# Kernel tuning notes

Measured on AMD Instinct MI355X. Metric: run time of the kernel, lower is better.

The kernel has to match this reference:

```python
import jax, jax.numpy as jnp
import numpy as np

NU, NI, D, E = 100000, 50000, 128, 500000


def setup_inputs() -> dict:
    key = jax.random.key(0)
    ks = jax.random.split(key, 10)
    s = 1.0 / np.sqrt(D)
    return {
        "feat_user": jax.random.normal(ks[0], (NU, D), jnp.float32),
        "feat_item": jax.random.normal(ks[1], (NI, D), jnp.float32),
        "W1": jax.random.normal(ks[2], (D, D), jnp.float32) * s,
        "b1": jnp.zeros((D,), jnp.float32),
        "W2": jax.random.normal(ks[3], (D, D), jnp.float32) * s,
        "b2": jnp.zeros((D,), jnp.float32),
        "norm_u2i": jax.random.uniform(ks[4], (E, 1), jnp.float32),
        "norm_i2u": jax.random.uniform(ks[5], (E, 1), jnp.float32),
        "edge_u2i_src": jax.random.randint(ks[6], (E,), 0, NU, jnp.int32),
        "edge_u2i_dst": jax.random.randint(ks[7], (E,), 0, NI, jnp.int32),
        "edge_i2u_src": jax.random.randint(ks[8], (E,), 0, NI, jnp.int32),
        "edge_i2u_dst": jax.random.randint(ks[9], (E,), 0, NU, jnp.int32),
    }


def reference(feat_user, feat_item, W1, b1, W2, b2, norm_u2i, norm_i2u,
              edge_u2i_src, edge_u2i_dst, edge_i2u_src, edge_i2u_dst):
    lin1 = lambda x: x @ W1 + b1
    lin2 = lambda x: x @ W2 + b2

    # self-loop etypes: copy_u(W1(feat)) summed over one self-edge per node
    h_user = lin1(feat_user)
    h_item = lin1(feat_item)

    # user -> item edges: norm * (W1(e_u) + W2(e_u * e_i)), scatter-sum to items
    su = feat_user[edge_u2i_src]            # [E, D]
    di = feat_item[edge_u2i_dst]            # [E, D]
    m_ui = norm_u2i * (lin1(su) + lin2(su * di))
    h_item = h_item + jax.ops.segment_sum(m_ui, edge_u2i_dst, num_segments=feat_item.shape[0])

    # item -> user edges
    si = feat_item[edge_i2u_src]
    du = feat_user[edge_i2u_dst]
    m_iu = norm_i2u * (lin1(si) + lin2(si * du))
    h_user = h_user + jax.ops.segment_sum(m_iu, edge_i2u_dst, num_segments=feat_user.shape[0])

    def finish(h):
        h = jax.nn.leaky_relu(h, 0.2)       # LeakyReLU(0.2); dropout p=0 is identity
        n = jnp.linalg.norm(h, axis=1, keepdims=True)
        return h / jnp.maximum(n, 1e-12)    # F.normalize(dim=1, p=2), eps=1e-12

    return finish(h_user), finish(h_item)
```

## Files before the change

### kernel.cpp

```cpp
#include <hip/hip_runtime.h>

#define DD 128
#define SCAN_TILE 1024
#define HS 132

typedef __attribute__((ext_vector_type(8))) short short8;
typedef __attribute__((ext_vector_type(4))) float f32x4;

__device__ inline unsigned short f2bf_rne(float f) {
    unsigned int u = __float_as_uint(f);
    unsigned int r = u + 0x7FFFu + ((u >> 16) & 1u);
    return (unsigned short)(r >> 16);
}
__device__ inline float bf2f(unsigned short h) {
    return __uint_as_float(((unsigned int)h) << 16);
}
__device__ inline void split2(float a, float b, unsigned int& hi, unsigned int& lo) {
    unsigned short ha = f2bf_rne(a), hb = f2bf_rne(b);
    float la = a - bf2f(ha), lb = b - bf2f(hb);
    hi = (unsigned int)ha | ((unsigned int)hb << 16);
    lo = (unsigned int)f2bf_rne(la) | ((unsigned int)f2bf_rne(lb) << 16);
}


__global__ __launch_bounds__(256) void count_kernel(
    const int* __restrict__ dst1, int E1, int* deg1,
    const int* __restrict__ dst2, int E2, int* deg2)
{
    int t = blockIdx.x * 256 + threadIdx.x;
    if (t < E1) {
        atomicAdd(deg1 + dst1[t], 1);
    } else if (t - E1 < E2) {
        atomicAdd(deg2 + dst2[t - E1], 1);
    }
}

__global__ __launch_bounds__(256) void scanA_kernel(
    const int* __restrict__ cur_i, int NI,
    const int* __restrict__ cur_u, int NU,
    int* bsum, int nb0)
{
    int b = blockIdx.x;
    const int* cur;
    int N, base;
    if (b < nb0) { cur = cur_i; N = NI; base = b * SCAN_TILE; }
    else         { cur = cur_u; N = NU; base = (b - nb0) * SCAN_TILE; }
    int t = threadIdx.x;
    int idx0 = base + t * 4;
    int s = 0;
    #pragma unroll
    for (int k = 0; k < 4; ++k) {
        int idx = idx0 + k;
        if (idx < N) s += cur[idx];
    }
    __shared__ int red[256];
    red[t] = s;
    __syncthreads();
    for (int o = 128; o >= 1; o >>= 1) {
        if (t < o) red[t] += red[t + o];
        __syncthreads();
    }
    if (t == 0) bsum[b] = red[0];
}

__device__ int block_exscan_inplace(int* a, int n)
{
    __shared__ int sh[256];
    int t = threadIdx.x;
    int carry = 0;
    for (int base = 0; base < n; base += 256) {
        int v = (base + t < n) ? a[base + t] : 0;
        sh[t] = v;
        __syncthreads();
        for (int off = 1; off < 256; off <<= 1) {
            int u = (t >= off) ? sh[t - off] : 0;
            __syncthreads();
            sh[t] += u;
            __syncthreads();
        }
        if (base + t < n) a[base + t] = carry + sh[t] - v;
        int csum = sh[255];
        __syncthreads();
        carry += csum;
    }
    return carry;
}

__global__ __launch_bounds__(256) void scanB_kernel(
    int* bsum, int nb0, int nb1,
    int* row_i, int NI, int* row_u, int NU)
{
    int tot0 = block_exscan_inplace(bsum, nb0);
    __syncthreads();
    int tot1 = block_exscan_inplace(bsum + nb0, nb1);
    if (threadIdx.x == 0) {
        row_i[NI] = tot0;
        row_u[NU] = tot1;
    }
}

__global__ __launch_bounds__(256) void scanC_kernel(
    int* cur_i, int* row_i, int NI,
    int* cur_u, int* row_u, int NU,
    const int* __restrict__ bsum, int nb0)
{
    int b = blockIdx.x;
    int off = bsum[b];
    int* cur; int* row;
    int N, base;
    if (b < nb0) { cur = cur_i; row = row_i; N = NI; base = b * SCAN_TILE; }
    else         { cur = cur_u; row = row_u; N = NU; base = (b - nb0) * SCAN_TILE; }
    int t = threadIdx.x;
    int idx0 = base + t * 4;
    int v[4];
    int s = 0;
    #pragma unroll
    for (int k = 0; k < 4; ++k) {
        int idx = idx0 + k;
        v[k] = (idx < N) ? cur[idx] : 0;
        s += v[k];
    }
    __shared__ int sh[256];
    sh[t] = s;
    __syncthreads();
    for (int o = 1; o < 256; o <<= 1) {
        int u = (t >= o) ? sh[t - o] : 0;
        __syncthreads();
        sh[t] += u;
        __syncthreads();
    }
    int run = off + sh[t] - s;
    #pragma unroll
    for (int k = 0; k < 4; ++k) {
        int idx = idx0 + k;
        if (idx < N) {
            row[idx] = run;
            cur[idx] = run;
            run += v[k];
        }
    }
}

__global__ __launch_bounds__(256) void fill_pg_kernel(
    const int* __restrict__ dst1, const int* __restrict__ src1,
    const float* __restrict__ norm1, int E1, int* cur1, int* ss1, float* ns1,
    const int* __restrict__ dst2, const int* __restrict__ src2,
    const float* __restrict__ norm2, int E2, int* cur2, int* ss2, float* ns2)
{
    int t = blockIdx.x * 256 + threadIdx.x;
    if (t < E1) {
        int pos = atomicAdd(cur1 + dst1[t], 1);
        ss1[pos] = src1[t];
        ns1[pos] = norm1[t];
    } else if (t - E1 < E2) {
        int e = t - E1;
        int pos = atomicAdd(cur2 + dst2[e], 1);
        ss2[pos] = src2[e];
        ns2[pos] = norm2[e];
    }
}


__global__ __launch_bounds__(256) void scatter_kernel(
    const float* __restrict__ feat_src,
    const int* __restrict__ src,
    const int* __restrict__ dst,
    const float* __restrict__ norm,
    float* agg,
    float* ssum,
    int E)
{
    int gw = (int)((blockIdx.x * 256u + threadIdx.x) >> 6);
    int lane = threadIdx.x & 63;
    if (gw >= E) return;
    int si = src[gw];
    int di = dst[gw];
    float nv = norm[gw];
    float2 v = *(const float2*)(feat_src + (size_t)si * DD + lane * 2);
    float* ap = agg + (size_t)di * DD + lane * 2;
    unsafeAtomicAdd(ap,     v.x * nv);
    unsafeAtomicAdd(ap + 1, v.y * nv);
    if (lane == 0) unsafeAtomicAdd(ssum + di, nv);
}

__global__ __launch_bounds__(256) void wprep_kernel(
    const float* __restrict__ W1, const float* __restrict__ W2,
    unsigned short* wfrag)
{
    int t = blockIdx.x * 256 + threadIdx.x;
    if (t >= 4096) return;
    int lane = t & 63;
    int cf   = (t >> 6) & 7;
    int ksm  = (t >> 9) & 3;
    int mat  = t >> 11;
    const float* W = mat ? W2 : W1;
    int g = lane >> 4, c = lane & 15;
    int n = cf * 16 + c;
    unsigned int hi[4], lo[4];
    #pragma unroll
    for (int p = 0; p < 4; ++p) {
        int k0 = ksm * 32 + g * 8 + p * 2;
        float v0 = W[(size_t)k0 * DD + n];
        float v1 = W[(size_t)(k0 + 1) * DD + n];
        split2(v0, v1, hi[p], lo[p]);
    }
    unsigned short* dh = wfrag + (size_t)mat * 32768
                       + ((size_t)(ksm * 8 + cf) * 64 + lane) * 8;
    unsigned short* dl = dh + 16384;
    *(uint4*)dh = make_uint4(hi[0], hi[1], hi[2], hi[3]);
    *(uint4*)dl = make_uint4(lo[0], lo[1], lo[2], lo[3]);
}

__global__ __launch_bounds__(256) void fused_kernel(
    const float* __restrict__ feat_user, const float* __restrict__ feat_item,
    const int* __restrict__ row_u, const int* __restrict__ ss2,
    const float* __restrict__ ns2, int NU, int nbU,
    const int* __restrict__ row_i, const int* __restrict__ ss1,
    const float* __restrict__ ns1, int NI,
    const unsigned short* __restrict__ wfrag,
    const float* __restrict__ b1, const float* __restrict__ b2,
    float* out_base)
{
    __shared__ __align__(16) unsigned short Ah[32 * 256];
    __shared__ __align__(16) unsigned short Al[32 * 256];
    __shared__ float sst[32];

    const float *featO, *featS, *ns;
    const int *row, *ss;
    float* out;
    int row0, nrows;
    if ((int)blockIdx.x < nbU) {
        featO = feat_user; featS = feat_item; row = row_u; ss = ss2; ns = ns2;
        out = out_base; row0 = blockIdx.x * 32; nrows = NU;
    } else {
        featO = feat_item; featS = feat_user; row = row_i; ss = ss1; ns = ns1;
        out = out_base + (size_t)NU * DD;
        row0 = (blockIdx.x - nbU) * 32; nrows = NI;
    }

    int t = threadIdx.x;
    int w = t >> 6;
    int lane = t & 63;
    char* pAh = (char*)Ah;
    char* pAl = (char*)Al;

    for (int rr = 0; rr < 8; ++rr) {
        int r = w * 8 + rr;
        int grow = row0 + r;
        float2 acc = {0.f, 0.f};
        float sn = 0.f;
        float2 f2 = {0.f, 0.f};
        if (grow < nrows) {
            f2 = *(const float2*)(featO + (size_t)grow * DD + lane * 2);
            int beg = row[grow], end = row[grow + 1];
            int j = beg;
            for (; j + 4 <= end; j += 4) {
                int s0 = ss[j], s1 = ss[j + 1], s2 = ss[j + 2], s3 = ss[j + 3];
                float n0 = ns[j],     n1 = ns[j + 1];
                float n2 = ns[j + 2], n3 = ns[j + 3];
                float2 v0 = *(const float2*)(featS + (size_t)s0 * DD + lane * 2);
                float2 v1 = *(const float2*)(featS + (size_t)s1 * DD + lane * 2);
                float2 v2 = *(const float2*)(featS + (size_t)s2 * DD + lane * 2);
                float2 v3 = *(const float2*)(featS + (size_t)s3 * DD + lane * 2);
                acc.x += n0 * v0.x + n1 * v1.x + n2 * v2.x + n3 * v3.x;
                acc.y += n0 * v0.y + n1 * v1.y + n2 * v2.y + n3 * v3.y;
                sn += n0 + n1 + n2 + n3;
            }
            for (; j < end; ++j) {
                int s0 = ss[j];
                float n0 = ns[j];
                float2 v0 = *(const float2*)(featS + (size_t)s0 * DD + lane * 2);
                acc.x += n0 * v0.x;
                acc.y += n0 * v0.y;
                sn += n0;
            }
        }
        float x0 = f2.x + acc.x, x1 = f2.y + acc.y;
        float y0 = f2.x * acc.x, y1 = f2.y * acc.y;
        unsigned int xh, xl, yh, yl;
        split2(x0, x1, xh, xl);
        split2(y0, y1, yh, yl);
        int swz = (r & 7) << 4;
        int rb = r * 512;
        int xo = rb + ((4 * lane) ^ swz);
        int yo = rb + ((256 + 4 * lane) ^ swz);
        *(unsigned int*)(pAh + xo) = xh;
        *(unsigned int*)(pAl + xo) = xl;
        *(unsigned int*)(pAh + yo) = yh;
        *(unsigned int*)(pAl + yo) = yl;
        if (lane == 0) sst[r] = sn;
    }
    __syncthreads();

    int r16 = lane & 15, g = lane >> 4;
    f32x4 acc00 = {0.f,0.f,0.f,0.f}, acc01 = {0.f,0.f,0.f,0.f};
    f32x4 acc10 = {0.f,0.f,0.f,0.f}, acc11 = {0.f,0.f,0.f,0.f};
    const char* cAh = (const char*)Ah;
    const char* cAl = (const char*)Al;
    int swzA = (r16 & 7) << 4;
    int ob0 = r16 * 512;
    int ob1 = (r16 + 16) * 512;

    #pragma unroll 2
    for (int ks = 0; ks < 8; ++ks) {
        int kb = ks * 64 + g * 16;
        int offx = kb ^ swzA;
        short8 a0h = *(const short8*)(cAh + ob0 + offx);
        short8 a0l = *(const short8*)(cAl + ob0 + offx);
        short8 a1h = *(const short8*)(cAh + ob1 + offx);
        short8 a1l = *(const short8*)(cAl + ob1 + offx);
        int mat = ks >> 2, ksm = ks & 3;
        const unsigned short* ph = wfrag + (size_t)mat * 32768;
        const unsigned short* pl = ph + 16384;
        int bo0 = ((ksm * 8 + w * 2) * 64 + lane) * 8;
        int bo1 = bo0 + 512;
        short8 b0h = *(const short8*)(ph + bo0);
        short8 b0l = *(const short8*)(pl + bo0);
        short8 b1h = *(const short8*)(ph + bo1);
        short8 b1l = *(const short8*)(pl + bo1);
        acc00 = __builtin_amdgcn_mfma_f32_16x16x32_bf16(a0h, b0h, acc00, 0, 0, 0);
        acc00 = __builtin_amdgcn_mfma_f32_16x16x32_bf16(a0h, b0l, acc00, 0, 0, 0);
        acc00 = __builtin_amdgcn_mfma_f32_16x16x32_bf16(a0l, b0h, acc00, 0, 0, 0);
        acc01 = __builtin_amdgcn_mfma_f32_16x16x32_bf16(a0h, b1h, acc01, 0, 0, 0);
        acc01 = __builtin_amdgcn_mfma_f32_16x16x32_bf16(a0h, b1l, acc01, 0, 0, 0);
        acc01 = __builtin_amdgcn_mfma_f32_16x16x32_bf16(a0l, b1h, acc01, 0, 0, 0);
        acc10 = __builtin_amdgcn_mfma_f32_16x16x32_bf16(a1h, b0h, acc10, 0, 0, 0);
        acc10 = __builtin_amdgcn_mfma_f32_16x16x32_bf16(a1h, b0l, acc10, 0, 0, 0);
        acc10 = __builtin_amdgcn_mfma_f32_16x16x32_bf16(a1l, b0h, acc10, 0, 0, 0);
        acc11 = __builtin_amdgcn_mfma_f32_16x16x32_bf16(a1h, b1h, acc11, 0, 0, 0);
        acc11 = __builtin_amdgcn_mfma_f32_16x16x32_bf16(a1h, b1l, acc11, 0, 0, 0);
        acc11 = __builtin_amdgcn_mfma_f32_16x16x32_bf16(a1l, b1h, acc11, 0, 0, 0);
    }
    __syncthreads();

    float* hbuf = (float*)Ah;
    #pragma unroll
    for (int j = 0; j < 4; ++j) {
        int rA = g * 4 + j;
        hbuf[rA * HS        + (w * 32 + r16)]      = acc00[j];
        hbuf[rA * HS        + (w * 32 + 16 + r16)] = acc01[j];
        hbuf[(16 + rA) * HS + (w * 32 + r16)]      = acc10[j];
        hbuf[(16 + rA) * HS + (w * 32 + 16 + r16)] = acc11[j];
    }
    __syncthreads();

    int c0 = t & 63, c1 = c0 + 64, rg = t >> 6;
    float b1c0 = b1[c0], b1c1 = b1[c1];
    float b2c0 = b2[c0], b2c1 = b2[c1];
    #pragma unroll
    for (int rr = 0; rr < 8; ++rr) {
        int lr = rg * 8 + rr;
        int row_ = row0 + lr;
        if (row_ < nrows) {
            float s = sst[lr];
            float h0 = hbuf[lr * HS + c0] + (1.0f + s) * b1c0 + s * b2c0;
            float h1 = hbuf[lr * HS + c1] + (1.0f + s) * b1c1 + s * b2c1;
            h0 = h0 >= 0.f ? h0 : 0.2f * h0;
            h1 = h1 >= 0.f ? h1 : 0.2f * h1;
            float loc = h0 * h0 + h1 * h1;
            #pragma unroll
            for (int m = 32; m >= 1; m >>= 1) loc += __shfl_xor(loc, m, 64);
            float inv = 1.0f / fmaxf(sqrtf(loc), 1e-12f);
            __builtin_nontemporal_store(h0 * inv, out + (size_t)row_ * DD + c0);
            __builtin_nontemporal_store(h1 * inv, out + (size_t)row_ * DD + c1);
        }
    }
}


__global__ __launch_bounds__(256) void finish_kernel(
    const float* __restrict__ feat,
    const float* agg,
    const float* __restrict__ ssum,
    const float* __restrict__ W1,
    const float* __restrict__ b1,
    const float* __restrict__ W2,
    const float* __restrict__ b2,
    float* out,
    int nrows)
{
    __shared__ float xs[32][DD];
    __shared__ float ys[32][DD];
    int row0 = blockIdx.x * 32;
    int tid = threadIdx.x;

    for (int i = tid; i < 32 * (DD / 4); i += 256) {
        int r = i >> 5;
        int c4 = (i & 31) * 4;
        int row = row0 + r;
        if (row < nrows) {
            float4 f = *(const float4*)(feat + (size_t)row * DD + c4);
            float4 a = *(const float4*)(agg  + (size_t)row * DD + c4);
            float4 x, y;
            x.x = f.x + a.x; x.y = f.y + a.y; x.z = f.z + a.z; x.w = f.w + a.w;
            y.x = f.x * a.x; y.y = f.y * a.y; y.z = f.z * a.z; y.w = f.w * a.w;
            *(float4*)&xs[r][c4] = x;
            *(float4*)&ys[r][c4] = y;
        }
    }
    __syncthreads();

    int c0 = tid & 63;
    int rg = tid >> 6;
    int c1 = c0 + 64;

    float acc[8][2] = {{0.f,0.f},{0.f,0.f},{0.f,0.f},{0.f,0.f},
                       {0.f,0.f},{0.f,0.f},{0.f,0.f},{0.f,0.f}};
    for (int k = 0; k < DD; k += 4) {
        float w1a[4], w1b[4], w2a[4], w2b[4];
        #pragma unroll
        for (int kk = 0; kk < 4; ++kk) {
            const float* wr1 = W1 + (size_t)(k + kk) * DD;
            const float* wr2 = W2 + (size_t)(k + kk) * DD;
            w1a[kk] = wr1[c0]; w1b[kk] = wr1[c1];
            w2a[kk] = wr2[c0]; w2b[kk] = wr2[c1];
        }
        #pragma unroll
        for (int r = 0; r < 8; ++r) {
            float4 xv = *(const float4*)&xs[rg * 8 + r][k];
            float4 yv = *(const float4*)&ys[rg * 8 + r][k];
            acc[r][0] += xv.x*w1a[0] + xv.y*w1a[1] + xv.z*w1a[2] + xv.w*w1a[3]
                       + yv.x*w2a[0] + yv.y*w2a[1] + yv.z*w2a[2] + yv.w*w2a[3];
            acc[r][1] += xv.x*w1b[0] + xv.y*w1b[1] + xv.z*w1b[2] + xv.w*w1b[3]
                       + yv.x*w2b[0] + yv.y*w2b[1] + yv.z*w2b[2] + yv.w*w2b[3];
        }
    }

    float b1c0 = b1[c0], b1c1 = b1[c1];
    float b2c0 = b2[c0], b2c1 = b2[c1];

    #pragma unroll
    for (int r = 0; r < 8; ++r) {
        int row = row0 + rg * 8 + r;
        if (row < nrows) {
            float s = ssum[row];
            float h0 = acc[r][0] + (1.0f + s) * b1c0 + s * b2c0;
            float h1 = acc[r][1] + (1.0f + s) * b1c1 + s * b2c1;
            h0 = h0 >= 0.f ? h0 : 0.2f * h0;
            h1 = h1 >= 0.f ? h1 : 0.2f * h1;
            float loc = h0 * h0 + h1 * h1;
            #pragma unroll
            for (int m = 32; m >= 1; m >>= 1) loc += __shfl_xor(loc, m, 64);
            float inv = 1.0f / fmaxf(sqrtf(loc), 1e-12f);
            out[(size_t)row * DD + c0] = h0 * inv;
            out[(size_t)row * DD + c1] = h1 * inv;
        }
    }
}

extern "C" void kernel_launch(void* const* d_in, const int* in_sizes, int n_in,
                              void* d_out, int out_size, void* d_ws, size_t ws_size,
                              hipStream_t stream) {
    const float* feat_user = (const float*)d_in[0];
    const float* feat_item = (const float*)d_in[1];
    const float* W1        = (const float*)d_in[2];
    const float* b1        = (const float*)d_in[3];
    const float* W2        = (const float*)d_in[4];
    const float* b2        = (const float*)d_in[5];
    const float* norm_u2i  = (const float*)d_in[6];
    const float* norm_i2u  = (const float*)d_in[7];
    const int* eus = (const int*)d_in[8];
    const int* eud = (const int*)d_in[9];
    const int* eis = (const int*)d_in[10];
    const int* eid = (const int*)d_in[11];

    int NU = in_sizes[0] / DD;
    int NI = in_sizes[1] / DD;
    int E1 = in_sizes[8];
    int E2 = in_sizes[10];
    float* out = (float*)d_out;

    int nb0 = (NI + SCAN_TILE - 1) / SCAN_TILE;
    int nb1 = (NU + SCAN_TILE - 1) / SCAN_TILE;
    int nbU = (NU + 31) / 32;
    int nbI = (NI + 31) / 32;

    size_t wfrag_bytes = 131072;
    size_t need_pg   = wfrag_bytes +
                       ((size_t)3 * NU + 3 * NI + 2 * E1 + 2 * E2 + 2
                        + nb0 + nb1) * sizeof(int);

    int eb = (int)(((long long)E1 + E2 + 255) / 256);

    if (ws_size >= need_pg) {
        unsigned short* wfrag = (unsigned short*)d_ws;
        int* cur_i = (int*)((char*)d_ws + wfrag_bytes);
        int* cur_u = cur_i + NI;
        int* row_i = cur_u + NU;
        int* row_u = row_i + NI + 1;
        int* ss1   = row_u + NU + 1;
        int* ss2   = ss1 + E1;
        float* ns1 = (float*)(ss2 + E2);
        float* ns2 = ns1 + E1;
        int* bsum  = (int*)(ns2 + E2);

        wprep_kernel<<<16, 256, 0, stream>>>(W1, W2, wfrag);

        hipMemsetAsync(cur_i, 0, (size_t)(NI + NU) * sizeof(int), stream);

        count_kernel<<<eb, 256, 0, stream>>>(eud, E1, cur_i, eid, E2, cur_u);
        scanA_kernel<<<nb0 + nb1, 256, 0, stream>>>(cur_i, NI, cur_u, NU,
                                                    bsum, nb0);
        scanB_kernel<<<1, 256, 0, stream>>>(bsum, nb0, nb1,
                                            row_i, NI, row_u, NU);
        scanC_kernel<<<nb0 + nb1, 256, 0, stream>>>(cur_i, row_i, NI,
                                                    cur_u, row_u, NU,
                                                    bsum, nb0);
        fill_pg_kernel<<<eb, 256, 0, stream>>>(
            eud, eus, norm_u2i, E1, cur_i, ss1, ns1,
            eid, eis, norm_i2u, E2, cur_u, ss2, ns2);

        fused_kernel<<<nbU + nbI, 256, 0, stream>>>(
            feat_user, feat_item,
            row_u, ss2, ns2, NU, nbU,
            row_i, ss1, ns1, NI,
            wfrag, b1, b2, out);
    } else {
        float* agg_user = out;
        float* agg_item = out + (size_t)NU * DD;
        float* s_user = (float*)d_ws;
        float* s_item = s_user + NU;

        hipMemsetAsync(out, 0, (size_t)out_size * sizeof(float), stream);
        hipMemsetAsync(d_ws, 0, (size_t)(NU + NI) * sizeof(float), stream);

        int b1n = (int)(((long long)E1 * 64 + 255) / 256);
        scatter_kernel<<<b1n, 256, 0, stream>>>(feat_user, eus, eud, norm_u2i,
                                                agg_item, s_item, E1);
        int b2n = (int)(((long long)E2 * 64 + 255) / 256);
        scatter_kernel<<<b2n, 256, 0, stream>>>(feat_item, eis, eid, norm_i2u,
                                                agg_user, s_user, E2);

        finish_kernel<<<nbU, 256, 0, stream>>>(
            feat_user, agg_user, s_user, W1, b1, W2, b2, out, NU);
        finish_kernel<<<nbI, 256, 0, stream>>>(
            feat_item, agg_item, s_item, W1, b1, W2, b2,
            out + (size_t)NU * DD, NI);
    }
}
```

Before: 418.6 us.

## Halve fused block rows, pack edge src/norm pairs, merge wprep into count

The fused gather+MFMA kernel now processes 16 rows per block instead of 32. This halves shared memory and accumulator registers and doubles the block count, aiming for better occupancy and latency hiding in the gather phase. Edge source indices and norms are interleaved into one int2 array, so each edge is fetched with a single 8-byte load. The weight-fragment prep is folded into the degree-count kernel to save one launch. In exchange, weight fragments are reloaded by twice as many blocks and each MFMA pass does less work per B-fragment load.

Result: faster. 379.6 us (-9.3%).

```diff
diff --git a/kernel.cpp b/kernel.cpp
--- a/kernel.cpp
+++ b/kernel.cpp
@@ -3,6 +3,7 @@
 #define DD 128
 #define SCAN_TILE 1024
 #define HS 132
+#define FR 16
 
 typedef __attribute__((ext_vector_type(8))) short short8;
 typedef __attribute__((ext_vector_type(4))) float f32x4;
@@ -22,12 +23,38 @@
     lo = (unsigned int)f2bf_rne(la) | ((unsigned int)f2bf_rne(lb) << 16);
 }
 
-
-__global__ __launch_bounds__(256) void count_kernel(
+__global__ __launch_bounds__(256) void count_wprep_kernel(
     const int* __restrict__ dst1, int E1, int* deg1,
-    const int* __restrict__ dst2, int E2, int* deg2)
-{
-    int t = blockIdx.x * 256 + threadIdx.x;
+    const int* __restrict__ dst2, int E2, int* deg2,
+    const float* __restrict__ W1, const float* __restrict__ W2,
+    unsigned short* wfrag)
+{
+    int b = blockIdx.x;
+    if (b < 16) {
+        int t = b * 256 + threadIdx.x;
+        int lane = t & 63;
+        int cf   = (t >> 6) & 7;
+        int ksm  = (t >> 9) & 3;
+        int mat  = t >> 11;
+        const float* W = mat ? W2 : W1;
+        int g = lane >> 4, c = lane & 15;
+        int n = cf * 16 + c;
+        unsigned int hi[4], lo[4];
+        #pragma unroll
+        for (int p = 0; p < 4; ++p) {
+            int k0 = ksm * 32 + g * 8 + p * 2;
+            float v0 = W[(size_t)k0 * DD + n];
+            float v1 = W[(size_t)(k0 + 1) * DD + n];
+            split2(v0, v1, hi[p], lo[p]);
+        }
+        unsigned short* dh = wfrag + (size_t)mat * 32768
+                           + ((size_t)(ksm * 8 + cf) * 64 + lane) * 8;
+        unsigned short* dl = dh + 16384;
+        *(uint4*)dh = make_uint4(hi[0], hi[1], hi[2], hi[3]);
+        *(uint4*)dl = make_uint4(lo[0], lo[1], lo[2], lo[3]);
+        return;
+    }
+    int t = (b - 16) * 256 + threadIdx.x;
     if (t < E1) {
         atomicAdd(deg1 + dst1[t], 1);
     } else if (t - E1 < E2) {
@@ -143,20 +170,18 @@
 
 __global__ __launch_bounds__(256) void fill_pg_kernel(
     const int* __restrict__ dst1, const int* __restrict__ src1,
-    const float* __restrict__ norm1, int E1, int* cur1, int* ss1, float* ns1,
+    const float* __restrict__ norm1, int E1, int* cur1, int2* esn1,
     const int* __restrict__ dst2, const int* __restrict__ src2,
-    const float* __restrict__ norm2, int E2, int* cur2, int* ss2, float* ns2)
+    const float* __restrict__ norm2, int E2, int* cur2, int2* esn2)
 {
     int t = blockIdx.x * 256 + threadIdx.x;
     if (t < E1) {
         int pos = atomicAdd(cur1 + dst1[t], 1);
-        ss1[pos] = src1[t];
-        ns1[pos] = norm1[t];
+        esn1[pos] = make_int2(src1[t], __float_as_int(norm1[t]));
     } else if (t - E1 < E2) {
         int e = t - E1;
         int pos = atomicAdd(cur2 + dst2[e], 1);
-        ss2[pos] = src2[e];
-        ns2[pos] = norm2[e];
+        esn2[pos] = make_int2(src2[e], __float_as_int(norm2[e]));
     }
 }
 
@@ -183,69 +208,40 @@
     if (lane == 0) unsafeAtomicAdd(ssum + di, nv);
 }
 
-__global__ __launch_bounds__(256) void wprep_kernel(
-    const float* __restrict__ W1, const float* __restrict__ W2,
-    unsigned short* wfrag)
-{
-    int t = blockIdx.x * 256 + threadIdx.x;
-    if (t >= 4096) return;
-    int lane = t & 63;
-    int cf   = (t >> 6) & 7;
-    int ksm  = (t >> 9) & 3;
-    int mat  = t >> 11;
-    const float* W = mat ? W2 : W1;
-    int g = lane >> 4, c = lane & 15;
-    int n = cf * 16 + c;
-    unsigned int hi[4], lo[4];
-    #pragma unroll
-    for (int p = 0; p < 4; ++p) {
-        int k0 = ksm * 32 + g * 8 + p * 2;
-        float v0 = W[(size_t)k0 * DD + n];
-        float v1 = W[(size_t)(k0 + 1) * DD + n];
-        split2(v0, v1, hi[p], lo[p]);
-    }
-    unsigned short* dh = wfrag + (size_t)mat * 32768
-                       + ((size_t)(ksm * 8 + cf) * 64 + lane) * 8;
-    unsigned short* dl = dh + 16384;
-    *(uint4*)dh = make_uint4(hi[0], hi[1], hi[2], hi[3]);
-    *(uint4*)dl = make_uint4(lo[0], lo[1], lo[2], lo[3]);
-}
-
 __global__ __launch_bounds__(256) void fused_kernel(
     const float* __restrict__ feat_user, const float* __restrict__ feat_item,
-    const int* __restrict__ row_u, const int* __restrict__ ss2,
-    const float* __restrict__ ns2, int NU, int nbU,
-    const int* __restrict__ row_i, const int* __restrict__ ss1,
-    const float* __restrict__ ns1, int NI,
+    const int* __restrict__ row_u, const int2* __restrict__ esnU,
+    int NU, int nbU,
+    const int* __restrict__ row_i, const int2* __restrict__ esnI, int NI,
     const unsigned short* __restrict__ wfrag,
     const float* __restrict__ b1, const float* __restrict__ b2,
     float* out_base)
 {
-    __shared__ __align__(16) unsigned short Ah[32 * 256];
-    __shared__ __align__(16) unsigned short Al[32 * 256];
-    __shared__ float sst[32];
-
-    const float *featO, *featS, *ns;
-    const int *row, *ss;
+    __shared__ __align__(16) char smem[FR * 512 * 2];
+    __shared__ float sst[FR];
+
+    const float *featO, *featS;
+    const int *row;
+    const int2 *esn;
     float* out;
     int row0, nrows;
     if ((int)blockIdx.x < nbU) {
-        featO = feat_user; featS = feat_item; row = row_u; ss = ss2; ns = ns2;
-        out = out_base; row0 = blockIdx.x * 32; nrows = NU;
+        featO = feat_user; featS = feat_item; row = row_u; esn = esnU;
+        out = out_base; row0 = blockIdx.x * FR; nrows = NU;
     } else {
-        featO = feat_item; featS = feat_user; row = row_i; ss = ss1; ns = ns1;
+        featO = feat_item; featS = feat_user; row = row_i; esn = esnI;
         out = out_base + (size_t)NU * DD;
-        row0 = (blockIdx.x - nbU) * 32; nrows = NI;
+        row0 = (blockIdx.x - nbU) * FR; nrows = NI;
     }
 
     int t = threadIdx.x;
     int w = t >> 6;
     int lane = t & 63;
-    char* pAh = (char*)Ah;
-    char* pAl = (char*)Al;
-
-    for (int rr = 0; rr < 8; ++rr) {
-        int r = w * 8 + rr;
+    char* pAh = smem;
+    char* pAl = smem + FR * 512;
+
+    for (int rr = 0; rr < 4; ++rr) {
+        int r = w * 4 + rr;
         int grow = row0 + r;
         float2 acc = {0.f, 0.f};
         float sn = 0.f;
@@ -255,21 +251,22 @@
             int beg = row[grow], end = row[grow + 1];
             int j = beg;
             for (; j + 4 <= end; j += 4) {
-                int s0 = ss[j], s1 = ss[j + 1], s2 = ss[j + 2], s3 = ss[j + 3];
-                float n0 = ns[j],     n1 = ns[j + 1];
-                float n2 = ns[j + 2], n3 = ns[j + 3];
-                float2 v0 = *(const float2*)(featS + (size_t)s0 * DD + lane * 2);
-                float2 v1 = *(const float2*)(featS + (size_t)s1 * DD + lane * 2);
-                float2 v2 = *(const float2*)(featS + (size_t)s2 * DD + lane * 2);
-                float2 v3 = *(const float2*)(featS + (size_t)s3 * DD + lane * 2);
+                int2 e0 = esn[j],     e1 = esn[j + 1];
+                int2 e2 = esn[j + 2], e3 = esn[j + 3];
+                float2 v0 = *(const float2*)(featS + (size_t)e0.x * DD + lane * 2);
+                float2 v1 = *(const float2*)(featS + (size_t)e1.x * DD + lane * 2);
+                float2 v2 = *(const float2*)(featS + (size_t)e2.x * DD + lane * 2);
+                float2 v3 = *(const float2*)(featS + (size_t)e3.x * DD + lane * 2);
+                float n0 = __int_as_float(e0.y), n1 = __int_as_float(e1.y);
+                float n2 = __int_as_float(e2.y), n3 = __int_as_float(e3.y);
                 acc.x += n0 * v0.x + n1 * v1.x + n2 * v2.x + n3 * v3.x;
                 acc.y += n0 * v0.y + n1 * v1.y + n2 * v2.y + n3 * v3.y;
                 sn += n0 + n1 + n2 + n3;
             }
             for (; j < end; ++j) {
-                int s0 = ss[j];
-                float n0 = ns[j];
-                float2 v0 = *(const float2*)(featS + (size_t)s0 * DD + lane * 2);
+                int2 e0 = esn[j];
+                float n0 = __int_as_float(e0.y);
+                float2 v0 = *(const float2*)(featS + (size_t)e0.x * DD + lane * 2);
                 acc.x += n0 * v0.x;
                 acc.y += n0 * v0.y;
                 sn += n0;
@@ -293,22 +290,17 @@
     __syncthreads();
 
     int r16 = lane & 15, g = lane >> 4;
-    f32x4 acc00 = {0.f,0.f,0.f,0.f}, acc01 = {0.f,0.f,0.f,0.f};
-    f32x4 acc10 = {0.f,0.f,0.f,0.f}, acc11 = {0.f,0.f,0.f,0.f};
-    const char* cAh = (const char*)Ah;
-    const char* cAl = (const char*)Al;
+    f32x4 acc0 = {0.f,0.f,0.f,0.f}, acc1 = {0.f,0.f,0.f,0.f};
+    const char* cAh = (const char*)pAh;
+    const char* cAl = (const char*)pAl;
     int swzA = (r16 & 7) << 4;
     int ob0 = r16 * 512;
-    int ob1 = (r16 + 16) * 512;
 
     #pragma unroll 2
     for (int ks = 0; ks < 8; ++ks) {
-        int kb = ks * 64 + g * 16;
-        int offx = kb ^ swzA;
+        int offx = (ks * 64 + g * 16) ^ swzA;
         short8 a0h = *(const short8*)(cAh + ob0 + offx);
         short8 a0l = *(const short8*)(cAl + ob0 + offx);
-        short8 a1h = *(const short8*)(cAh + ob1 + offx);
-        short8 a1l = *(const short8*)(cAl + ob1 + offx);
         int mat = ks >> 2, ksm = ks & 3;
         const unsigned short* ph = wfrag + (size_t)mat * 32768;
         const unsigned short* pl = ph + 16384;
@@ -318,29 +310,21 @@
         short8 b0l = *(const short8*)(pl + bo0);
         short8 b1h = *(const short8*)(ph + bo1);
         short8 b1l = *(const short8*)(pl + bo1);
-        acc00 = __builtin_amdgcn_mfma_f32_16x16x32_bf16(a0h, b0h, acc00, 0, 0, 0);
-        acc00 = __builtin_amdgcn_mfma_f32_16x16x32_bf16(a0h, b0l, acc00, 0, 0, 0);
-        acc00 = __builtin_amdgcn_mfma_f32_16x16x32_bf16(a0l, b0h, acc00, 0, 0, 0);
-        acc01 = __builtin_amdgcn_mfma_f32_16x16x32_bf16(a0h, b1h, acc01, 0, 0, 0);
-        acc01 = __builtin_amdgcn_mfma_f32_16x16x32_bf16(a0h, b1l, acc01, 0, 0, 0);
-        acc01 = __builtin_amdgcn_mfma_f32_16x16x32_bf16(a0l, b1h, acc01, 0, 0, 0);
-        acc10 = __builtin_amdgcn_mfma_f32_16x16x32_bf16(a1h, b0h, acc10, 0, 0, 0);
-        acc10 = __builtin_amdgcn_mfma_f32_16x16x32_bf16(a1h, b0l, acc10, 0, 0, 0);
-        acc10 = __builtin_amdgcn_mfma_f32_16x16x32_bf16(a1l, b0h, acc10, 0, 0, 0);
-        acc11 = __builtin_amdgcn_mfma_f32_16x16x32_bf16(a1h, b1h, acc11, 0, 0, 0);
-        acc11 = __builtin_amdgcn_mfma_f32_16x16x32_bf16(a1h, b1l, acc11, 0, 0, 0);
-        acc11 = __builtin_amdgcn_mfma_f32_16x16x32_bf16(a1l, b1h, acc11, 0, 0, 0);
-    }
-    __syncthreads();
-
-    float* hbuf = (float*)Ah;
+        acc0 = __builtin_amdgcn_mfma_f32_16x16x32_bf16(a0h, b0h, acc0, 0, 0, 0);
+        acc0 = __builtin_amdgcn_mfma_f32_16x16x32_bf16(a0h, b0l, acc0, 0, 0, 0);
+        acc0 = __builtin_amdgcn_mfma_f32_16x16x32_bf16(a0l, b0h, acc0, 0, 0, 0);
+        acc1 = __builtin_amdgcn_mfma_f32_16x16x32_bf16(a0h, b1h, acc1, 0, 0, 0);
+        acc1 = __builtin_amdgcn_mfma_f32_16x16x32_bf16(a0h, b1l, acc1, 0, 0, 0);
+        acc1 = __builtin_amdgcn_mfma_f32_16x16x32_bf16(a0l, b1h, acc1, 0, 0, 0);
+    }
+    __syncthreads();
+
+    float* hbuf = (float*)smem;
     #pragma unroll
     for (int j = 0; j < 4; ++j) {
         int rA = g * 4 + j;
-        hbuf[rA * HS        + (w * 32 + r16)]      = acc00[j];
-        hbuf[rA * HS        + (w * 32 + 16 + r16)] = acc01[j];
-        hbuf[(16 + rA) * HS + (w * 32 + r16)]      = acc10[j];
-        hbuf[(16 + rA) * HS + (w * 32 + 16 + r16)] = acc11[j];
+        hbuf[rA * HS + (w * 32 + r16)]      = acc0[j];
+        hbuf[rA * HS + (w * 32 + 16 + r16)] = acc1[j];
     }
     __syncthreads();
 
@@ -348,8 +332,8 @@
     float b1c0 = b1[c0], b1c1 = b1[c1];
     float b2c0 = b2[c0], b2c1 = b2[c1];
     #pragma unroll
-    for (int rr = 0; rr < 8; ++rr) {
-        int lr = rg * 8 + rr;
+    for (int rr = 0; rr < 4; ++rr) {
+        int lr = rg * 4 + rr;
         int row_ = row0 + lr;
         if (row_ < nrows) {
             float s = sst[lr];
@@ -472,11 +456,11 @@
 
     int nb0 = (NI + SCAN_TILE - 1) / SCAN_TILE;
     int nb1 = (NU + SCAN_TILE - 1) / SCAN_TILE;
-    int nbU = (NU + 31) / 32;
-    int nbI = (NI + 31) / 32;
+    int nbU = (NU + FR - 1) / FR;
+    int nbI = (NI + FR - 1) / FR;
 
     size_t wfrag_bytes = 131072;
-    size_t need_pg   = wfrag_bytes +
+    size_t need_pg   = wfrag_bytes + 64  +
                        ((size_t)3 * NU + 3 * NI + 2 * E1 + 2 * E2 + 2
                         + nb0 + nb1) * sizeof(int);
 
@@ -488,17 +472,15 @@
         int* cur_u = cur_i + NI;
         int* row_i = cur_u + NU;
         int* row_u = row_i + NI + 1;
-        int* ss1   = row_u + NU + 1;
-        int* ss2   = ss1 + E1;
-        float* ns1 = (float*)(ss2 + E2);
-        float* ns2 = ns1 + E1;
-        int* bsum  = (int*)(ns2 + E2);
-
-        wprep_kernel<<<16, 256, 0, stream>>>(W1, W2, wfrag);
+        int* pend  = row_u + NU + 1;
+        int2* esn1 = (int2*)(((uintptr_t)pend + 15) & ~(uintptr_t)15);
+        int2* esn2 = esn1 + E1;
+        int* bsum  = (int*)(esn2 + E2);
 
         hipMemsetAsync(cur_i, 0, (size_t)(NI + NU) * sizeof(int), stream);
 
-        count_kernel<<<eb, 256, 0, stream>>>(eud, E1, cur_i, eid, E2, cur_u);
+        count_wprep_kernel<<<16 + eb, 256, 0, stream>>>(
+            eud, E1, cur_i, eid, E2, cur_u, W1, W2, wfrag);
         scanA_kernel<<<nb0 + nb1, 256, 0, stream>>>(cur_i, NI, cur_u, NU,
                                                     bsum, nb0);
         scanB_kernel<<<1, 256, 0, stream>>>(bsum, nb0, nb1,
@@ -507,13 +489,13 @@
                                                     cur_u, row_u, NU,
                                                     bsum, nb0);
         fill_pg_kernel<<<eb, 256, 0, stream>>>(
-            eud, eus, norm_u2i, E1, cur_i, ss1, ns1,
-            eid, eis, norm_i2u, E2, cur_u, ss2, ns2);
+            eud, eus, norm_u2i, E1, cur_i, esn1,
+            eid, eis, norm_i2u, E2, cur_u, esn2);
 
         fused_kernel<<<nbU + nbI, 256, 0, stream>>>(
             feat_user, feat_item,
-            row_u, ss2, ns2, NU, nbU,
-            row_i, ss1, ns1, NI,
+            row_u, esn2, NU, nbU,
+            row_i, esn1, NI,
             wfrag, b1, b2, out);
     } else {
         float* agg_user = out;
@@ -531,9 +513,9 @@
         scatter_kernel<<<b2n, 256, 0, stream>>>(feat_item, eis, eid, norm_i2u,
                                                 agg_user, s_user, E2);
 
-        finish_kernel<<<nbU, 256, 0, stream>>>(
+        finish_kernel<<<(NU + 31) / 32, 256, 0, stream>>>(
             feat_user, agg_user, s_user, W1, b1, W2, b2, out, NU);
-        finish_kernel<<<nbI, 256, 0, stream>>>(
+        finish_kernel<<<(NI + 31) / 32, 256, 0, stream>>>(
             feat_item, agg_item, s_item, W1, b1, W2, b2,
             out + (size_t)NU * DD, NI);
     }
```
